# Performance work log

Hardware: AMD Instinct MI355X
Metric: run time of the kernel (lower is better)

The kernel has to match this reference:

```python
import jax, jax.numpy as jnp
import numpy as np

B, C, T, S = 128, 64, 8192, 16

def setup_inputs() -> dict:
    key = jax.random.key(0)
    k1, k2, k3, k4 = jax.random.split(key, 4)
    x = jax.random.normal(k1, (B, C, T), dtype=jnp.float32)
    subj_idx = jax.random.randint(k2, (B,), 0, S)
    # per-subject 1x1 conv == per-subject [C, C] matrix + bias.
    # (original identity-inits; we use identity + small noise so the op is non-trivial)
    W = jnp.eye(C, dtype=jnp.float32)[None] + 0.02 * jax.random.normal(k3, (S, C, C), dtype=jnp.float32)
    b = 0.02 * jax.random.normal(k4, (S, C), dtype=jnp.float32)
    return {"x": x, "subj_idx": subj_idx, "W": W, "b": b}

def reference(x, subj_idx, W, b):
    # Hard routing: gather each sample's subject weight, then batched 1x1 conv.
    Wb = W[subj_idx]            # [B, C_out, C_in]
    bb = b[subj_idx]            # [B, C_out]
    # out[b, o, t] = sum_c Wb[b, o, c] * x[b, c, t] + bb[b, o]
    return jnp.einsum('boc,bct->bot', Wb, x) + bb[:, :, None]
```

## Files before the change

### kernel.cpp

```cpp
#include <hip/hip_runtime.h>
#include <hip/hip_bf16.h>


typedef __attribute__((ext_vector_type(8))) short  bf16x8;
typedef __attribute__((ext_vector_type(16))) float f32x16;

namespace {
constexpr int Cdim  = 64;
constexpr int Tdim  = 8192;
constexpr int TT    = 256;
constexpr int BLOCK = 256;
}

static __device__ __forceinline__ short f2bf(float f) {
    return (short)__builtin_bit_cast(unsigned short, __float2bfloat16(f));
}

__global__ __launch_bounds__(BLOCK, 2)
void subject_layers_r10(const float* __restrict__ x,
                        const int*   __restrict__ subj,
                        const float* __restrict__ W,
                        const float* __restrict__ bias,
                        float*       __restrict__ out) {
    __shared__ float tile[Cdim * TT];

    const int b    = blockIdx.y;
    const int tb   = blockIdx.x;
    const int tid  = threadIdx.x;
    const int wave = tid >> 6;
    const int lane = tid & 63;
    const int hi   = lane >> 5;
    const int ln   = lane & 31;
    const int s    = subj[b];

    const size_t xbase = (size_t)b * Cdim * Tdim + (size_t)tb * TT;

    #pragma unroll
    for (int g = 0; g < 16; ++g) {
        const int row = g * 4 + wave;
        __builtin_amdgcn_global_load_lds(
            (const __attribute__((address_space(1))) unsigned int*)
                (x + xbase + (size_t)row * Tdim + lane * 4),
            (__attribute__((address_space(3))) unsigned int*)
                (&tile[row * TT]),
            16, 0, 0);
    }

    bf16x8 afrag[2][4];
    const float* Wb = W + (size_t)s * Cdim * Cdim;
    #pragma unroll
    for (int ot = 0; ot < 2; ++ot) {
        #pragma unroll
        for (int kb = 0; kb < 4; ++kb) {
            const float* ap = Wb + (size_t)(ot * 32 + ln) * Cdim + kb * 16 + hi * 8;
            const float4 a0 = *reinterpret_cast<const float4*>(ap);
            const float4 a1 = *reinterpret_cast<const float4*>(ap + 4);
            bf16x8 f;
            f[0] = f2bf(a0.x); f[1] = f2bf(a0.y); f[2] = f2bf(a0.z); f[3] = f2bf(a0.w);
            f[4] = f2bf(a1.x); f[5] = f2bf(a1.y); f[6] = f2bf(a1.z); f[7] = f2bf(a1.w);
            afrag[ot][kb] = f;
        }
    }

    f32x16 bini[2];
    const float* bb = bias + (size_t)s * Cdim;
    #pragma unroll
    for (int ot = 0; ot < 2; ++ot)
        #pragma unroll
        for (int r = 0; r < 16; ++r)
            bini[ot][r] = bb[ot * 32 + (r & 3) + 8 * (r >> 2) + 4 * hi];

    __syncthreads();

    float* ob = out + xbase;
    #pragma unroll
    for (int st = 0; st < 2; ++st) {
        const int col = wave * 64 + st * 32 + ln;

        bf16x8 bfrag[4];
        #pragma unroll
        for (int kb = 0; kb < 4; ++kb) {
            bf16x8 f;
            #pragma unroll
            for (int j = 0; j < 8; ++j)
                f[j] = f2bf(tile[(kb * 16 + hi * 8 + j) * TT + col]);
            bfrag[kb] = f;
        }

        #pragma unroll
        for (int ot = 0; ot < 2; ++ot) {
            f32x16 acc = bini[ot];
            #pragma unroll
            for (int kb = 0; kb < 4; ++kb)
                acc = __builtin_amdgcn_mfma_f32_32x32x16_bf16(
                    afrag[ot][kb], bfrag[kb], acc, 0, 0, 0);
            #pragma unroll
            for (int r = 0; r < 16; ++r)
                ob[(size_t)(ot * 32 + (r & 3) + 8 * (r >> 2) + 4 * hi) * Tdim + col]
                    = acc[r];
        }
    }
}

extern "C" void kernel_launch(void* const* d_in, const int* in_sizes, int n_in,
                              void* d_out, int out_size, void* d_ws, size_t ws_size,
                              hipStream_t stream) {
    const float* x    = (const float*)d_in[0];
    const int*   subj = (const int*)  d_in[1];
    const float* W    = (const float*)d_in[2];
    const float* bias = (const float*)d_in[3];
    float*       out  = (float*)d_out;

    const int B = in_sizes[1];
    dim3 grid(Tdim / TT, B);
    dim3 block(BLOCK);
    hipLaunchKernelGGL(subject_layers_r10, grid, block, 0, stream,
                       x, subj, W, bias, out);
}
```

Measured before the change: 104.5 us.

## Split channel load into two halves to overlap second load with first MFMAs

The 64-channel input tile is now loaded in two 32-channel halves into separate LDS buffers. The first half's partial GEMM (K=0..31) runs while the second half's async global-to-LDS loads are in flight, and the remaining K steps plus stores follow after a second barrier. This hides part of the load latency behind compute. In exchange there is an extra barrier and more live accumulator registers (four f32x16 accumulators per thread), which may pressure occupancy. The kernel is largely memory-bound, so the achievable overlap is limited.

```diff
diff --git a/kernel.cpp b/kernel.cpp
--- a/kernel.cpp
+++ b/kernel.cpp
@@ -17,12 +17,13 @@
 }
 
 __global__ __launch_bounds__(BLOCK, 2)
-void subject_layers_r10(const float* __restrict__ x,
+void subject_layers_r12(const float* __restrict__ x,
                         const int*   __restrict__ subj,
                         const float* __restrict__ W,
                         const float* __restrict__ bias,
                         float*       __restrict__ out) {
-    __shared__ float tile[Cdim * TT];
+    __shared__ float tA[32 * TT];
+    __shared__ float tB[32 * TT];
 
     const int b    = blockIdx.y;
     const int tb   = blockIdx.x;
@@ -36,13 +37,13 @@
     const size_t xbase = (size_t)b * Cdim * Tdim + (size_t)tb * TT;
 
     #pragma unroll
-    for (int g = 0; g < 16; ++g) {
+    for (int g = 0; g < 8; ++g) {
         const int row = g * 4 + wave;
         __builtin_amdgcn_global_load_lds(
             (const __attribute__((address_space(1))) unsigned int*)
                 (x + xbase + (size_t)row * Tdim + lane * 4),
             (__attribute__((address_space(3))) unsigned int*)
-                (&tile[row * TT]),
+                (&tA[row * TT]),
             16, 0, 0);
     }
 
@@ -62,13 +63,53 @@
         }
     }
 
-    f32x16 bini[2];
-    const float* bb = bias + (size_t)s * Cdim;
+    f32x16 acc[2][2];
+    {
+        const float* bb = bias + (size_t)s * Cdim;
+        #pragma unroll
+        for (int ot = 0; ot < 2; ++ot) {
+            f32x16 bi;
+            #pragma unroll
+            for (int r = 0; r < 16; ++r)
+                bi[r] = bb[ot * 32 + (r & 3) + 8 * (r >> 2) + 4 * hi];
+            acc[0][ot] = bi;
+            acc[1][ot] = bi;
+        }
+    }
+
+    __syncthreads();
+
     #pragma unroll
-    for (int ot = 0; ot < 2; ++ot)
+    for (int g = 0; g < 8; ++g) {
+        const int row = 32 + g * 4 + wave;
+        __builtin_amdgcn_global_load_lds(
+            (const __attribute__((address_space(1))) unsigned int*)
+                (x + xbase + (size_t)row * Tdim + lane * 4),
+            (__attribute__((address_space(3))) unsigned int*)
+                (&tB[(row - 32) * TT]),
+            16, 0, 0);
+    }
+
+    #pragma unroll
+    for (int st = 0; st < 2; ++st) {
+        const int col = wave * 64 + st * 32 + ln;
+        bf16x8 bfrag[2];
         #pragma unroll
-        for (int r = 0; r < 16; ++r)
-            bini[ot][r] = bb[ot * 32 + (r & 3) + 8 * (r >> 2) + 4 * hi];
+        for (int kb = 0; kb < 2; ++kb) {
+            bf16x8 f;
+            #pragma unroll
+            for (int j = 0; j < 8; ++j)
+                f[j] = f2bf(tA[(kb * 16 + hi * 8 + j) * TT + col]);
+            bfrag[kb] = f;
+        }
+        #pragma unroll
+        for (int ot = 0; ot < 2; ++ot) {
+            acc[st][ot] = __builtin_amdgcn_mfma_f32_32x32x16_bf16(
+                afrag[ot][0], bfrag[0], acc[st][ot], 0, 0, 0);
+            acc[st][ot] = __builtin_amdgcn_mfma_f32_32x32x16_bf16(
+                afrag[ot][1], bfrag[1], acc[st][ot], 0, 0, 0);
+        }
+    }
 
     __syncthreads();
 
@@ -76,28 +117,25 @@
     #pragma unroll
     for (int st = 0; st < 2; ++st) {
         const int col = wave * 64 + st * 32 + ln;
-
-        bf16x8 bfrag[4];
+        bf16x8 bfrag[2];
         #pragma unroll
-        for (int kb = 0; kb < 4; ++kb) {
+        for (int kb = 0; kb < 2; ++kb) {
             bf16x8 f;
             #pragma unroll
             for (int j = 0; j < 8; ++j)
-                f[j] = f2bf(tile[(kb * 16 + hi * 8 + j) * TT + col]);
+                f[j] = f2bf(tB[(kb * 16 + hi * 8 + j) * TT + col]);
             bfrag[kb] = f;
         }
-
         #pragma unroll
         for (int ot = 0; ot < 2; ++ot) {
-            f32x16 acc = bini[ot];
-            #pragma unroll
-            for (int kb = 0; kb < 4; ++kb)
-                acc = __builtin_amdgcn_mfma_f32_32x32x16_bf16(
-                    afrag[ot][kb], bfrag[kb], acc, 0, 0, 0);
+            acc[st][ot] = __builtin_amdgcn_mfma_f32_32x32x16_bf16(
+                afrag[ot][2], bfrag[0], acc[st][ot], 0, 0, 0);
+            acc[st][ot] = __builtin_amdgcn_mfma_f32_32x32x16_bf16(
+                afrag[ot][3], bfrag[1], acc[st][ot], 0, 0, 0);
             #pragma unroll
             for (int r = 0; r < 16; ++r)
                 ob[(size_t)(ot * 32 + (r & 3) + 8 * (r >> 2) + 4 * hi) * Tdim + col]
-                    = acc[r];
+                    = acc[st][ot][r];
         }
     }
 }
@@ -114,6 +152,6 @@
     const int B = in_sizes[1];
     dim3 grid(Tdim / TT, B);
     dim3 block(BLOCK);
-    hipLaunchKernelGGL(subject_layers_r10, grid, block, 0, stream,
+    hipLaunchKernelGGL(subject_layers_r12, grid, block, 0, stream,
                        x, subj, W, bias, out);
 }
```

Result: faster. 100.6 us (median of 2 runs) (-3.7%).

## Pipeline K-chunks of LDS tile with staged vmcnt waits and barriers

Applied to the files above, without the earlier changes.

Splits the global-to-LDS load of the x tile into four 16-row chunks. Each chunk's MFMAs start as soon as that chunk arrives, using partial s_waitcnt vmcnt counts and a barrier per chunk instead of one full wait. The loop order changes from per-column-strip to per-K-chunk, so all four accumulators (2 strips x 2 output tiles) stay live and results are stored at the end. This costs more accumulator registers and extra barriers. The hand-written vmcnt thresholds may also not isolate the intended loads, because the later W and bias global loads count toward the same counter.

```diff
diff --git a/kernel.cpp b/kernel.cpp
--- a/kernel.cpp
+++ b/kernel.cpp
@@ -17,7 +17,7 @@
 }
 
 __global__ __launch_bounds__(BLOCK, 2)
-void subject_layers_r10(const float* __restrict__ x,
+void subject_layers_r14(const float* __restrict__ x,
                         const int*   __restrict__ subj,
                         const float* __restrict__ W,
                         const float* __restrict__ bias,
@@ -36,14 +36,17 @@
     const size_t xbase = (size_t)b * Cdim * Tdim + (size_t)tb * TT;
 
     #pragma unroll
-    for (int g = 0; g < 16; ++g) {
-        const int row = g * 4 + wave;
-        __builtin_amdgcn_global_load_lds(
-            (const __attribute__((address_space(1))) unsigned int*)
-                (x + xbase + (size_t)row * Tdim + lane * 4),
-            (__attribute__((address_space(3))) unsigned int*)
-                (&tile[row * TT]),
-            16, 0, 0);
+    for (int q = 0; q < 4; ++q) {
+        #pragma unroll
+        for (int g = 0; g < 4; ++g) {
+            const int row = q * 16 + g * 4 + wave;
+            __builtin_amdgcn_global_load_lds(
+                (const __attribute__((address_space(1))) unsigned int*)
+                    (x + xbase + (size_t)row * Tdim + lane * 4),
+                (__attribute__((address_space(3))) unsigned int*)
+                    (&tile[row * TT]),
+                16, 0, 0);
+        }
     }
 
     bf16x8 afrag[2][4];
@@ -62,42 +65,54 @@
         }
     }
 
-    f32x16 bini[2];
-    const float* bb = bias + (size_t)s * Cdim;
-    #pragma unroll
-    for (int ot = 0; ot < 2; ++ot)
+    f32x16 acc[2][2];
+    {
+        const float* bb = bias + (size_t)s * Cdim;
         #pragma unroll
-        for (int r = 0; r < 16; ++r)
-            bini[ot][r] = bb[ot * 32 + (r & 3) + 8 * (r >> 2) + 4 * hi];
-
-    __syncthreads();
+        for (int ot = 0; ot < 2; ++ot) {
+            f32x16 bi;
+            #pragma unroll
+            for (int r = 0; r < 16; ++r)
+                bi[r] = bb[ot * 32 + (r & 3) + 8 * (r >> 2) + 4 * hi];
+            acc[0][ot] = bi;
+            acc[1][ot] = bi;
+        }
+    }
 
     float* ob = out + xbase;
     #pragma unroll
-    for (int st = 0; st < 2; ++st) {
-        const int col = wave * 64 + st * 32 + ln;
+    for (int q = 0; q < 4; ++q) {
+        if (q == 0)      asm volatile("s_waitcnt vmcnt(12)" ::: "memory");
+        else if (q == 1) asm volatile("s_waitcnt vmcnt(8)"  ::: "memory");
+        else if (q == 2) asm volatile("s_waitcnt vmcnt(4)"  ::: "memory");
+        else             asm volatile("s_waitcnt vmcnt(0)"  ::: "memory");
+        __builtin_amdgcn_s_barrier();
+        __builtin_amdgcn_sched_barrier(0);
 
-        bf16x8 bfrag[4];
         #pragma unroll
-        for (int kb = 0; kb < 4; ++kb) {
+        for (int st = 0; st < 2; ++st) {
+            const int col = wave * 64 + st * 32 + ln;
             bf16x8 f;
             #pragma unroll
             for (int j = 0; j < 8; ++j)
-                f[j] = f2bf(tile[(kb * 16 + hi * 8 + j) * TT + col]);
-            bfrag[kb] = f;
+                f[j] = f2bf(tile[(q * 16 + hi * 8 + j) * TT + col]);
+            #pragma unroll
+            for (int ot = 0; ot < 2; ++ot)
+                acc[st][ot] = __builtin_amdgcn_mfma_f32_32x32x16_bf16(
+                    afrag[ot][q], f, acc[st][ot], 0, 0, 0);
         }
 
-        #pragma unroll
-        for (int ot = 0; ot < 2; ++ot) {
-            f32x16 acc = bini[ot];
+        if (q == 3) {
             #pragma unroll
-            for (int kb = 0; kb < 4; ++kb)
-                acc = __builtin_amdgcn_mfma_f32_32x32x16_bf16(
-                    afrag[ot][kb], bfrag[kb], acc, 0, 0, 0);
-            #pragma unroll
-            for (int r = 0; r < 16; ++r)
-                ob[(size_t)(ot * 32 + (r & 3) + 8 * (r >> 2) + 4 * hi) * Tdim + col]
-                    = acc[r];
+            for (int st = 0; st < 2; ++st) {
+                const int col = wave * 64 + st * 32 + ln;
+                #pragma unroll
+                for (int ot = 0; ot < 2; ++ot)
+                    #pragma unroll
+                    for (int r = 0; r < 16; ++r)
+                        ob[(size_t)(ot * 32 + (r & 3) + 8 * (r >> 2) + 4 * hi) * Tdim + col]
+                            = acc[st][ot][r];
+            }
         }
     }
 }
@@ -114,6 +129,6 @@
     const int B = in_sizes[1];
     dim3 grid(Tdim / TT, B);
     dim3 block(BLOCK);
-    hipLaunchKernelGGL(subject_layers_r10, grid, block, 0, stream,
+    hipLaunchKernelGGL(subject_layers_r14, grid, block, 0, stream,
                        x, subj, W, bias, out);
 }
```

After: 104.8 us. No clear change (+0.3%).
